# Optimization experiments

Measured on AMD Instinct MI355X. Metric: run time of the kernel, lower is better.

Reference implementation:

```python
import jax, jax.numpy as jnp
import numpy as np

NS, NM, NR, H = 5000, 100000, 2000, 128
E_SM, E_RM, E_SIM, L = 2_000_000, 1_000_000, 2_000_000, 500_000
NUM_LAYERS = 4  # flattened: layer-0 sage convs 0..3, layer-1 sage convs 0..3 -> stacked [2,4,...]


def _seg_sum(x, idx, n):
    return jax.ops.segment_sum(x, idx, num_segments=n)


def sage_conv(x_src, x_dst, Wl, bl, Wr, src, dst, n_dst):
    # PyG SAGEConv: mean-aggregate neighbor features, lin_l (with bias), + lin_r(root, no bias)
    agg = _seg_sum(x_src[src], dst, n_dst)                      # [n_dst, H]
    cnt = _seg_sum(jnp.ones_like(src, dtype=x_src.dtype), dst, n_dst)
    mean = agg / jnp.maximum(cnt, 1.0)[:, None]
    return mean @ Wl + bl + x_dst @ Wr


def gcn_conv(x, W, b, src, dst, n):
    # PyG GCNConv: add self loops, symmetric normalization deg^-1/2 (deg over dst incl. self loops)
    loop = jnp.arange(n, dtype=src.dtype)
    src2 = jnp.concatenate([src, loop])
    dst2 = jnp.concatenate([dst, loop])
    deg = _seg_sum(jnp.ones_like(dst2, dtype=x.dtype), dst2, n)
    dinv = jnp.where(deg > 0, jax.lax.rsqrt(deg), 0.0)
    norm = dinv[src2] * dinv[dst2]                               # [E+n]
    xw = x @ W                                                   # [n, H]
    out = _seg_sum(xw[src2] * norm[:, None], dst2, n)
    return out + b


def setup_inputs() -> dict:
    key = jax.random.key(0)
    ks = jax.random.split(key, 20)
    s = 0.05
    inp = {
        "emb_srna": jax.random.normal(ks[0], (NS, H), jnp.float32) * s,
        "emb_mrna": jax.random.normal(ks[1], (NM, H), jnp.float32) * s,
        "emb_rbp": jax.random.normal(ks[2], (NR, H), jnp.float32) * s,
        # stacked SAGE params: [layer=2, rel=4, ...]; rel order:
        # 0: srna->mrna, 1: mrna->srna (rev), 2: rbp->mrna, 3: mrna->rbp (rev)
        "sage_Wl": jax.random.normal(ks[3], (2, 4, H, H), jnp.float32) * s,
        "sage_bl": jnp.zeros((2, 4, H), jnp.float32),
        "sage_Wr": jax.random.normal(ks[4], (2, 4, H, H), jnp.float32) * s,
        # stacked GCN params: [layer=2, rel=2 (sim, rev_sim), ...]
        "gcn_W": jax.random.normal(ks[5], (2, 2, H, H), jnp.float32) * s,
        "gcn_b": jnp.zeros((2, 2, H), jnp.float32),
        "src_sm": jax.random.randint(ks[6], (E_SM,), 0, NS),
        "dst_sm": jax.random.randint(ks[7], (E_SM,), 0, NM),
        "src_rm": jax.random.randint(ks[8], (E_RM,), 0, NR),
        "dst_rm": jax.random.randint(ks[9], (E_RM,), 0, NM),
        "src_sim": jax.random.randint(ks[10], (E_SIM,), 0, NM),
        "dst_sim": jax.random.randint(ks[11], (E_SIM,), 0, NM),
        "lbl_srna": jax.random.randint(ks[12], (L,), 0, NS),
        "lbl_mrna": jax.random.randint(ks[13], (L,), 0, NM),
        "lbl_rbp": jax.random.randint(ks[14], (L,), 0, NR),
    }
    return inp


def reference(emb_srna, emb_mrna, emb_rbp, sage_Wl, sage_bl, sage_Wr, gcn_W, gcn_b,
              src_sm, dst_sm, src_rm, dst_rm, src_sim, dst_sim,
              lbl_srna, lbl_mrna, lbl_rbp):
    x_s, x_m, x_r = emb_srna, emb_mrna, emb_rbp
    for l in range(2):
        m_new = (
            sage_conv(x_s, x_m, sage_Wl[l, 0], sage_bl[l, 0], sage_Wr[l, 0], src_sm, dst_sm, NM)
            + sage_conv(x_r, x_m, sage_Wl[l, 2], sage_bl[l, 2], sage_Wr[l, 2], src_rm, dst_rm, NM)
            + gcn_conv(x_m, gcn_W[l, 0], gcn_b[l, 0], src_sim, dst_sim, NM)
            + gcn_conv(x_m, gcn_W[l, 1], gcn_b[l, 1], dst_sim, src_sim, NM)
        )
        s_new = sage_conv(x_m, x_s, sage_Wl[l, 1], sage_bl[l, 1], sage_Wr[l, 1], dst_sm, src_sm, NS)
        r_new = sage_conv(x_m, x_r, sage_Wl[l, 3], sage_bl[l, 3], sage_Wr[l, 3], dst_rm, src_rm, NR)
        x_s, x_m, x_r = jax.nn.relu(s_new), jax.nn.relu(m_new), jax.nn.relu(r_new)
    feat_m = x_m[lbl_mrna]
    pred_srna_mrna = jnp.sum(x_s[lbl_srna] * feat_m, axis=-1)
    pred_rbp_mrna = jnp.sum(x_r[lbl_rbp] * feat_m, axis=-1)
    return (pred_srna_mrna, pred_rbp_mrna)
```

## Files before the change

kernel.cpp:

```cpp
#include <hip/hip_runtime.h>
#include <hip/hip_bf16.h>

#define NSN 5000
#define NMN 100000
#define NRN 2000
#define HDIM 128
#define ESM 2000000
#define ERM 1000000
#define ESIM 2000000
#define LBL 500000

#define CNT_TOTAL (4 * NMN + NSN + NRN)
#define POOL_TOTAL (2 * ESM + 2 * ERM + 2 * ESIM)
#define NBTOT 1222
#define WCAP 14336
#define MAXNODES 512
#define SR_TOTAL (NSN + NRN)

#define CAP0 12288
#define CAP1 8192
#define CAP2 7168
#define CAP3 9216
#define CAP4 12288
#define CAP5 12288
#define PB0 0
#define PB1 (PB0 + 196 * CAP0)
#define PB2 (PB1 + 313 * CAP1)
#define PB3 (PB2 + 196 * CAP2)
#define PB4 (PB3 + 125 * CAP3)
#define PB5 (PB4 + 196 * CAP4)

typedef short bf16x8 __attribute__((ext_vector_type(8)));
typedef float f32x4 __attribute__((ext_vector_type(4)));
typedef float f32x2 __attribute__((ext_vector_type(2)));

__device__ __forceinline__ unsigned short f2bf(float f) {
  unsigned u = __float_as_uint(f);
  unsigned r = (u + 0x7fffu + ((u >> 16) & 1u)) >> 16;
  return (unsigned short)r;
}
__device__ __forceinline__ float bf_lo(unsigned v) { return __uint_as_float(v << 16); }
__device__ __forceinline__ float bf_hi(unsigned v) { return __uint_as_float(v & 0xffff0000u); }
__device__ __forceinline__ unsigned pack2(float x, float y) {
  return (unsigned)f2bf(x) | ((unsigned)f2bf(y) << 16);
}
__device__ __forceinline__ void unpack8(uint4 v, float* f) {
  f[0] = bf_lo(v.x); f[1] = bf_hi(v.x);
  f[2] = bf_lo(v.y); f[3] = bf_hi(v.y);
  f[4] = bf_lo(v.z); f[5] = bf_hi(v.z);
  f[6] = bf_lo(v.w); f[7] = bf_hi(v.w);
}


__global__ void zero_int(int* __restrict__ p, int n) {
  int i = blockIdx.x * blockDim.x + threadIdx.x;
  if (i < n) p[i] = 0;
}

struct BInfo { int g; int ns; int ne; };
__device__ __forceinline__ BInfo binfo(int id) {
  BInfo bi;
  if (id < 196)       { int k = id;        bi.g = 0;                   bi.ns = k << 9; bi.ne = min(bi.ns + 512, NMN); }
  else if (id < 509)  { int k = id - 196;  bi.g = NMN;                 bi.ns = k << 4; bi.ne = min(bi.ns + 16,  NSN); }
  else if (id < 705)  { int k = id - 509;  bi.g = NMN + NSN;           bi.ns = k << 9; bi.ne = min(bi.ns + 512, NMN); }
  else if (id < 830)  { int k = id - 705;  bi.g = 2 * NMN + NSN;       bi.ns = k << 4; bi.ne = min(bi.ns + 16,  NRN); }
  else if (id < 1026) { int k = id - 830;  bi.g = 2 * NMN + NSN + NRN; bi.ns = k << 9; bi.ne = min(bi.ns + 512, NMN); }
  else                { int k = id - 1026; bi.g = 3 * NMN + NSN + NRN; bi.ns = k << 9; bi.ne = min(bi.ns + 512, NMN); }
  return bi;
}

__device__ __forceinline__ int pstart(int id) {
  if (id < 196)       return PB0 + id * CAP0;
  else if (id < 509)  return PB1 + (id - 196) * CAP1;
  else if (id < 705)  return PB2 + (id - 509) * CAP2;
  else if (id < 830)  return PB3 + (id - 705) * CAP3;
  else if (id < 1026) return PB4 + (id - 830) * CAP4;
  else                return PB5 + (id - 1026) * CAP5;
}

__global__ void init_pcur(int* __restrict__ bcur) {
  int id = blockIdx.x * blockDim.x + threadIdx.x;
  if (id < NBTOT) bcur[id] = pstart(id);
}

template <int SHF, int NBF, int SHR, int NBR>
__global__ __launch_bounds__(256) void multisplit(
    const int* __restrict__ a, const int* __restrict__ b, int n,
    int* __restrict__ bcur, int bb, int2* __restrict__ stage) {
  __shared__ int hist[NBF + NBR];
  __shared__ int gpos[NBF + NBR];
  int tid = threadIdx.x;
  int base = blockIdx.x * 4096;
  for (int k = tid; k < NBF + NBR; k += 256) hist[k] = 0;
  __syncthreads();
  int dv[16], sv[16];
#pragma unroll
  for (int j = 0; j < 16; j++) {
    int idx = base + j * 256 + tid;
    if (idx < n) {
      sv[j] = a[idx]; dv[j] = b[idx];
      atomicAdd(&hist[dv[j] >> SHF], 1);
      atomicAdd(&hist[NBF + (sv[j] >> SHR)], 1);
    } else {
      dv[j] = -1;
    }
  }
  __syncthreads();
  for (int k = tid; k < NBF + NBR; k += 256) {
    int c = hist[k];
    gpos[k] = c ? atomicAdd(&bcur[bb + k], c) : 0;
  }
  __syncthreads();
#pragma unroll
  for (int j = 0; j < 16; j++) {
    if (dv[j] >= 0) {
      int s1 = atomicAdd(&gpos[dv[j] >> SHF], 1);
      stage[s1] = make_int2(dv[j], sv[j]);
      int s2 = atomicAdd(&gpos[NBF + (sv[j] >> SHR)], 1);
      stage[s2] = make_int2(sv[j], dv[j]);
    }
  }
}

__global__ void scan_counts(const int* __restrict__ bcur, int* __restrict__ bstart,
                            int* __restrict__ off_sentinel) {
  __shared__ int buf[256];
  int t = threadIdx.x;
  int base = 0;
  for (int c0 = 0; c0 < NBTOT; c0 += 256) {
    int id = c0 + t;
    int v = (id < NBTOT) ? (bcur[id] - pstart(id)) : 0;
    buf[t] = v; __syncthreads();
    for (int o = 1; o < 256; o <<= 1) {
      int a = (t >= o) ? buf[t - o] : 0;
      __syncthreads();
      buf[t] += a;
      __syncthreads();
    }
    if (id < NBTOT) bstart[id] = buf[t] - v + base;
    base += buf[255];
    __syncthreads();
  }
  if (t == 0) { bstart[NBTOT] = base; *off_sentinel = base; }
}

__global__ __launch_bounds__(256) void scatter_bucket(
    const int2* __restrict__ stage, const int* __restrict__ bstart,
    int* __restrict__ cur, int* __restrict__ off, int* __restrict__ pool) {
  __shared__ int win[WCAP];
  __shared__ int hist[MAXNODES];
  __shared__ int part[256];
  int b = blockIdx.x;
  BInfo bi = binfo(b);
  int p0 = pstart(b);
  int d0 = bstart[b];
  int sz = bstart[b + 1] - d0;
  int nn = bi.ne - bi.ns;
  int t = threadIdx.x;
  for (int k = t; k < nn; k += 256) hist[k] = 0;
  __syncthreads();
  for (int k = t; k < sz; k += 256)
    atomicAdd(&hist[stage[p0 + k].x - bi.ns], 1);
  __syncthreads();
  int a0 = (2 * t < nn) ? hist[2 * t] : 0;
  int a1 = (2 * t + 1 < nn) ? hist[2 * t + 1] : 0;
  part[t] = a0 + a1;
  __syncthreads();
  for (int o = 1; o < 256; o <<= 1) {
    int a = (t >= o) ? part[t - o] : 0;
    __syncthreads();
    part[t] += a;
    __syncthreads();
  }
  int e0 = part[t] - a0 - a1;
  int e1 = e0 + a0;
  if (2 * t < nn)     { off[bi.g + bi.ns + 2 * t] = d0 + e0; hist[2 * t] = e0; }
  if (2 * t + 1 < nn) { off[bi.g + bi.ns + 2 * t + 1] = d0 + e1; hist[2 * t + 1] = e1; }
  __syncthreads();
  if (sz <= WCAP) {
    for (int k = t; k < sz; k += 256) {
      int2 pr = stage[p0 + k];
      int slot = atomicAdd(&hist[pr.x - bi.ns], 1);
      win[slot] = pr.y;
    }
    __syncthreads();
    for (int k = t; k < sz; k += 256) pool[d0 + k] = win[k];
  } else {
    for (int k = t; k < sz; k += 256) {
      int2 pr = stage[p0 + k];
      int slot = atomicAdd(&cur[bi.g + pr.x], 1);
      pool[d0 + hist[pr.x - bi.ns] + slot] = pr.y;
    }
  }
}

__global__ void compute_dinv(const int* __restrict__ off1, const int* __restrict__ off2,
                             float* __restrict__ dinv1, float* __restrict__ dinv2, int n) {
  int v = blockIdx.x * blockDim.x + threadIdx.x;
  if (v < n) {
    dinv1[v] = rsqrtf((float)(off1[v + 1] - off1[v] + 1));
    dinv2[v] = rsqrtf((float)(off2[v + 1] - off2[v] + 1));
  }
}

__global__ void trans_weights(const float* __restrict__ sWl, const float* __restrict__ sWr,
                              const float* __restrict__ gW, unsigned short* __restrict__ wt) {
  int i = blockIdx.x * blockDim.x + threadIdx.x;
  if (i >= 18 * 16384) return;
  int mat = i >> 14, l = mat / 9, slot = mat % 9;
  int idx = i & 16383, nn = idx >> 7, kk = idx & 127;
  int s_ = kk * 128 + nn;
  float v;
  if (slot < 4)      v = sWl[((l * 4 + slot) << 14) + s_];
  else if (slot < 6) v = gW[((l * 2 + (slot - 4)) << 14) + s_];
  else if (slot == 6) v = sWr[((l * 4 + 0) << 14) + s_] + sWr[((l * 4 + 2) << 14) + s_];
  else if (slot == 7) v = sWr[((l * 4 + 1) << 14) + s_];
  else                v = sWr[((l * 4 + 3) << 14) + s_];
  wt[i] = f2bf(v);
}

__global__ void prep_bias(const float* __restrict__ sbl, const float* __restrict__ gb,
                          float* __restrict__ biasM) {
  int i = threadIdx.x;
  int l = i >> 7, j = i & 127;
  biasM[i] = sbl[(l * 4 + 0) * 128 + j] + sbl[(l * 4 + 2) * 128 + j] +
             gb[(l * 2 + 0) * 128 + j] + gb[(l * 2 + 1) * 128 + j];
}

__global__ void cast_all(const float2* __restrict__ es, const float2* __restrict__ em,
                         const float2* __restrict__ er, unsigned* __restrict__ os,
                         unsigned* __restrict__ om, unsigned* __restrict__ orr) {
  int i = blockIdx.x * blockDim.x + threadIdx.x;
  if (i < NSN * 64) { float2 v = es[i]; os[i] = pack2(v.x, v.y); }
  if (i < NMN * 64) { float2 v = em[i]; om[i] = pack2(v.x, v.y); }
  if (i < NRN * 64) { float2 v = er[i]; orr[i] = pack2(v.x, v.y); }
}


template <bool GCN>
__device__ __forceinline__ f32x2 agg_list(const char* __restrict__ xb,
                                          const int* __restrict__ pool,
                                          const float* __restrict__ dinv,
                                          int s, int e, int l4) {
  f32x2 a0 = (f32x2)(0.f), a1 = (f32x2)(0.f);
  if (e <= s) return a0;
  for (int i0 = s; i0 < e; i0 += 64) {
    int cnt = min(64, e - i0);
    int pidx = min(i0 + (l4 >> 2), e - 1);
    int pv = pool[pidx];
    float dvv = 0.f;
    if (GCN) dvv = dinv[pv];
    int k = 0;
    for (; k + 16 <= cnt; k += 16) {
      unsigned vv[16];
      float sc[16];
#pragma unroll
      for (int j = 0; j < 16; j++) {
        int u = __builtin_amdgcn_readlane(pv, k + j);
        if (GCN)
          sc[j] = __uint_as_float(
              (unsigned)__builtin_amdgcn_readlane((int)__float_as_uint(dvv), k + j));
        vv[j] = *(const unsigned*)(xb + (((unsigned)u << 8) + (unsigned)l4));
      }
#pragma unroll
      for (int j = 0; j < 16; j++) {
        float m = GCN ? sc[j] : 1.0f;
        if (j & 1) {
          a1.x = fmaf(bf_lo(vv[j]), m, a1.x);
          a1.y = fmaf(bf_hi(vv[j]), m, a1.y);
        } else {
          a0.x = fmaf(bf_lo(vv[j]), m, a0.x);
          a0.y = fmaf(bf_hi(vv[j]), m, a0.y);
        }
      }
    }
    if (k < cnt) {
      unsigned vv[16];
      float sc[16];
#pragma unroll
      for (int j = 0; j < 16; j++) {
        int kk = min(k + j, cnt - 1);
        int u = __builtin_amdgcn_readlane(pv, kk);
        float m;
        if (k + j < cnt)
          m = GCN ? __uint_as_float(
                        (unsigned)__builtin_amdgcn_readlane((int)__float_as_uint(dvv), kk))
                  : 1.0f;
        else
          m = 0.0f;
        sc[j] = m;
        vv[j] = *(const unsigned*)(xb + (((unsigned)u << 8) + (unsigned)l4));
      }
#pragma unroll
      for (int j = 0; j < 16; j++) {
        if (j & 1) {
          a1.x = fmaf(bf_lo(vv[j]), sc[j], a1.x);
          a1.y = fmaf(bf_hi(vv[j]), sc[j], a1.y);
        } else {
          a0.x = fmaf(bf_lo(vv[j]), sc[j], a0.x);
          a0.y = fmaf(bf_hi(vv[j]), sc[j], a0.y);
        }
      }
    }
  }
  return a0 + a1;
}

__global__ __launch_bounds__(256) void agg_all(
    const unsigned* __restrict__ xs, const unsigned* __restrict__ xm,
    const unsigned* __restrict__ xr, const int* __restrict__ pool,
    const int* __restrict__ off_sm, const int* __restrict__ off_rm,
    const int* __restrict__ off_si, const int* __restrict__ off_si2,
    const int* __restrict__ off_ms, const int* __restrict__ off_mr,
    const float* __restrict__ dinv1, const float* __restrict__ dinv2,
    unsigned* __restrict__ aggA, unsigned* __restrict__ aggB,
    unsigned* __restrict__ aggC, unsigned* __restrict__ aggD,
    unsigned* __restrict__ aggS, unsigned* __restrict__ aggR) {
  int wv = blockIdx.x * 4 + (threadIdx.x >> 6);
  wv = __builtin_amdgcn_readfirstlane(wv);
  int l = threadIdx.x & 63;
  int l4 = l << 2;

  if (wv < SR_TOTAL) {
    int node;
    const int* offp;
    unsigned* outb;
    if (wv < NSN) { node = wv; offp = off_ms; outb = aggS; }
    else          { node = wv - NSN; offp = off_mr; outb = aggR; }
    int s = offp[node], e = offp[node + 1];
    f32x2 a = agg_list<false>((const char*)xm, pool, nullptr, s, e, l4);
    float inv = (e > s) ? 1.0f / (float)(e - s) : 0.0f;
    outb[(size_t)node * 64 + l] = pack2(a.x * inv, a.y * inv);
  } else {
    int w = wv - SR_TOTAL;
    int sA = off_sm[w],  eA = off_sm[w + 1];
    int sB = off_rm[w],  eB = off_rm[w + 1];
    int sC = off_si[w],  eC = off_si[w + 1];
    int sD = off_si2[w], eD = off_si2[w + 1];
    unsigned xv = xm[(size_t)w * 64 + l];
    float dw1 = dinv1[w], dw2_ = dinv2[w];

    {
      f32x2 a = agg_list<false>((const char*)xs, pool, nullptr, sA, eA, l4);
      float inv = (eA > sA) ? 1.0f / (float)(eA - sA) : 0.0f;
      aggA[(size_t)w * 64 + l] = pack2(a.x * inv, a.y * inv);
    }
    {
      f32x2 a = agg_list<false>((const char*)xr, pool, nullptr, sB, eB, l4);
      float inv = (eB > sB) ? 1.0f / (float)(eB - sB) : 0.0f;
      aggB[(size_t)w * 64 + l] = pack2(a.x * inv, a.y * inv);
    }
    {
      f32x2 a = agg_list<true>((const char*)xm, pool, dinv1, sC, eC, l4);
      float dsq = dw1 * dw1;
      float rx = a.x * dw1 + bf_lo(xv) * dsq;
      float ry = a.y * dw1 + bf_hi(xv) * dsq;
      aggC[(size_t)w * 64 + l] = pack2(rx, ry);
    }
    {
      f32x2 a = agg_list<true>((const char*)xm, pool, dinv2, sD, eD, l4);
      float dsq = dw2_ * dw2_;
      float rx = a.x * dw2_ + bf_lo(xv) * dsq;
      float ry = a.y * dw2_ + bf_hi(xv) * dsq;
      aggD[(size_t)w * 64 + l] = pack2(rx, ry);
    }
  }
}


#define LDA 136

__global__ __launch_bounds__(256) void gemm_mfma(
    const unsigned short* __restrict__ a0, const unsigned short* __restrict__ w0,
    const unsigned short* __restrict__ a1, const unsigned short* __restrict__ w1,
    const unsigned short* __restrict__ a2, const unsigned short* __restrict__ w2,
    const unsigned short* __restrict__ a3, const unsigned short* __restrict__ w3,
    const unsigned short* __restrict__ a4, const unsigned short* __restrict__ w4,
    const float* __restrict__ bias, unsigned short* __restrict__ out, int n) {
  __shared__ __align__(16) unsigned short As[64 * LDA];
  __shared__ __align__(16) unsigned short Ws[128 * LDA];

  int tid = threadIdx.x;
  int w = tid >> 6, lane = tid & 63;
  int q = lane >> 4, c = lane & 15;
  int r0 = blockIdx.x * 64;

  const unsigned short* Ap[5] = {a0, a1, a2, a3, a4};
  const unsigned short* Wp[5] = {w0, w1, w2, w3, w4};

  float bias_v[8];
#pragma unroll
  for (int n0 = 0; n0 < 8; n0++) bias_v[n0] = bias[n0 * 16 + c];

  f32x4 acc[8];
#pragma unroll
  for (int n0 = 0; n0 < 8; n0++) acc[n0] = (f32x4){0.f, 0.f, 0.f, 0.f};

  for (int p = 0; p < 5; p++) {
    if (!Ap[p]) continue;
    __syncthreads();
    for (int j = tid; j < 2048; j += 256) {
      int row = j >> 4, colc = (j & 15) * 8;
      *(uint4*)&Ws[row * LDA + colc] = *(const uint4*)(Wp[p] + row * 128 + colc);
    }
    for (int j = tid; j < 1024; j += 256) {
      int row = j >> 4, colc = (j & 15) * 8;
      uint4 v = make_uint4(0u, 0u, 0u, 0u);
      if (r0 + row < n) v = *(const uint4*)(Ap[p] + (size_t)(r0 + row) * 128 + colc);
      *(uint4*)&As[row * LDA + colc] = v;
    }
    __syncthreads();

    int arow = (w * 16 + c) * LDA;
#pragma unroll
    for (int k0 = 0; k0 < 128; k0 += 32) {
      bf16x8 af = *(const bf16x8*)&As[arow + k0 + q * 8];
#pragma unroll
      for (int n0 = 0; n0 < 8; n0++) {
        bf16x8 bfv = *(const bf16x8*)&Ws[(n0 * 16 + c) * LDA + k0 + q * 8];
        acc[n0] = __builtin_amdgcn_mfma_f32_16x16x32_bf16(af, bfv, acc[n0], 0, 0, 0);
      }
    }
  }

  __syncthreads();
#pragma unroll
  for (int n0 = 0; n0 < 8; n0++) {
#pragma unroll
    for (int reg = 0; reg < 4; reg++) {
      float v = acc[n0][reg] + bias_v[n0];
      v = fmaxf(v, 0.f);
      As[(w * 16 + q * 4 + reg) * LDA + n0 * 16 + c] = f2bf(v);
    }
  }
  __syncthreads();
  for (int j = tid; j < 1024; j += 256) {
    int row = j >> 4, colc = (j & 15) * 8;
    if (r0 + row < n)
      *(uint4*)(out + (size_t)(r0 + row) * 128 + colc) = *(const uint4*)&As[row * LDA + colc];
  }
}


__global__ void dots_kernel(const unsigned* __restrict__ xs, const unsigned* __restrict__ xm,
                            const unsigned* __restrict__ xr, const int* __restrict__ ls,
                            const int* __restrict__ lm, const int* __restrict__ lr,
                            float* __restrict__ out) {
  int wv = (blockIdx.x * blockDim.x + threadIdx.x) >> 6;
  int lane = threadIdx.x & 63;
  int q = lane >> 4, h = lane & 15;
  int i = wv * 4 + q;
  if (i >= LBL) return;
  int im = lm[i], is = ls[i], ir = lr[i];
  uint4 mv = *(const uint4*)(xm + (size_t)im * 64 + h * 4);
  uint4 sv = *(const uint4*)(xs + (size_t)is * 64 + h * 4);
  uint4 rv = *(const uint4*)(xr + (size_t)ir * 64 + h * 4);
  float fm[8], fs[8], fr[8];
  unpack8(mv, fm); unpack8(sv, fs); unpack8(rv, fr);
  float p1 = 0.f, p2 = 0.f;
#pragma unroll
  for (int j = 0; j < 8; j++) { p1 = fmaf(fs[j], fm[j], p1); p2 = fmaf(fr[j], fm[j], p2); }
#pragma unroll
  for (int m = 1; m < 16; m <<= 1) {
    p1 += __shfl_xor(p1, m, 64);
    p2 += __shfl_xor(p2, m, 64);
  }
  if (h == 0) { out[i] = p1; out[LBL + i] = p2; }
}


extern "C" void kernel_launch(void* const* d_in, const int* in_sizes, int n_in,
                              void* d_out, int out_size, void* d_ws, size_t ws_size,
                              hipStream_t stream) {
  const float* emb_s = (const float*)d_in[0];
  const float* emb_m = (const float*)d_in[1];
  const float* emb_r = (const float*)d_in[2];
  const float* sWl = (const float*)d_in[3];
  const float* sbl = (const float*)d_in[4];
  const float* sWr = (const float*)d_in[5];
  const float* gW  = (const float*)d_in[6];
  const float* gb  = (const float*)d_in[7];
  const int* src_sm  = (const int*)d_in[8];
  const int* dst_sm  = (const int*)d_in[9];
  const int* src_rm  = (const int*)d_in[10];
  const int* dst_rm  = (const int*)d_in[11];
  const int* src_sim = (const int*)d_in[12];
  const int* dst_sim = (const int*)d_in[13];
  const int* lbl_s = (const int*)d_in[14];
  const int* lbl_m = (const int*)d_in[15];
  const int* lbl_r = (const int*)d_in[16];
  float* out = (float*)d_out;

  char* p = (char*)d_ws;
  auto alloc = [&](size_t bytes) -> char* {
    char* r = p;
    p += (bytes + 255) & ~(size_t)255;
    return r;
  };

  int* cnt_base = (int*)alloc(sizeof(int) * CNT_TOTAL);

  int* off_base = (int*)alloc(sizeof(int) * (CNT_TOTAL + 1));
  int* off_sm  = off_base;
  int* off_ms  = off_sm + NMN;
  int* off_rm  = off_ms + NSN;
  int* off_mr  = off_rm + NMN;
  int* off_si  = off_mr + NRN;
  int* off_si2 = off_si + NMN;

  int* bstart = (int*)alloc(sizeof(int) * 1280);
  int* bcur   = (int*)alloc(sizeof(int) * 1280);
  int* pool = (int*)alloc(sizeof(int) * POOL_TOTAL);

  float* dinv1 = (float*)alloc(sizeof(float) * NMN);
  float* dinv2 = (float*)alloc(sizeof(float) * NMN);

  unsigned* xsb = (unsigned*)alloc(sizeof(unsigned) * (size_t)NSN * 64);
  unsigned* xmb = (unsigned*)alloc(sizeof(unsigned) * (size_t)NMN * 64);
  unsigned* xrb = (unsigned*)alloc(sizeof(unsigned) * (size_t)NRN * 64);
  unsigned* xs0 = (unsigned*)alloc(sizeof(unsigned) * (size_t)NSN * 64);
  unsigned* xs1 = (unsigned*)alloc(sizeof(unsigned) * (size_t)NSN * 64);
  unsigned* xm0 = (unsigned*)alloc(sizeof(unsigned) * (size_t)NMN * 64);
  unsigned* xm1 = (unsigned*)alloc(sizeof(unsigned) * (size_t)NMN * 64);
  unsigned* xr0 = (unsigned*)alloc(sizeof(unsigned) * (size_t)NRN * 64);
  unsigned* xr1 = (unsigned*)alloc(sizeof(unsigned) * (size_t)NRN * 64);
  unsigned* aggA = (unsigned*)alloc(sizeof(unsigned) * (size_t)NMN * 64);
  unsigned* aggB = (unsigned*)alloc(sizeof(unsigned) * (size_t)NMN * 64);
  unsigned* aggC = (unsigned*)alloc(sizeof(unsigned) * (size_t)NMN * 64);
  unsigned* aggD = (unsigned*)alloc(sizeof(unsigned) * (size_t)NMN * 64);
  unsigned* aggS = (unsigned*)alloc(sizeof(unsigned) * (size_t)NSN * 64);
  unsigned* aggR = (unsigned*)alloc(sizeof(unsigned) * (size_t)NRN * 64);

  unsigned short* wt = (unsigned short*)alloc(sizeof(unsigned short) * 18 * 16384);
  float* biasM = (float*)alloc(sizeof(float) * 2 * 128);

  int2* stage = (int2*)aggA;

  auto WT = [&](int l, int slot) -> const unsigned short* {
    return wt + (((size_t)l * 9 + slot) << 14);
  };

  init_pcur<<<(NBTOT + 255) / 256, 256, 0, stream>>>(bcur);
  multisplit<9, 196, 4, 313><<<(ESM + 4095) / 4096, 256, 0, stream>>>(
      src_sm, dst_sm, ESM, bcur, 0, stage);
  multisplit<9, 196, 4, 125><<<(ERM + 4095) / 4096, 256, 0, stream>>>(
      src_rm, dst_rm, ERM, bcur, 509, stage);
  multisplit<9, 196, 9, 196><<<(ESIM + 4095) / 4096, 256, 0, stream>>>(
      src_sim, dst_sim, ESIM, bcur, 830, stage);
  scan_counts<<<1, 256, 0, stream>>>(bcur, bstart, off_base + CNT_TOTAL);
  zero_int<<<(CNT_TOTAL + 255) / 256, 256, 0, stream>>>(cnt_base, CNT_TOTAL);
  scatter_bucket<<<NBTOT, 256, 0, stream>>>(stage, bstart, cnt_base, off_base, pool);

  compute_dinv<<<(NMN + 255) / 256, 256, 0, stream>>>(off_si, off_si2, dinv1, dinv2, NMN);
  trans_weights<<<(18 * 16384 + 255) / 256, 256, 0, stream>>>(sWl, sWr, gW, wt);
  prep_bias<<<1, 256, 0, stream>>>(sbl, gb, biasM);
  cast_all<<<(NMN * 64 + 255) / 256, 256, 0, stream>>>((const float2*)emb_s, (const float2*)emb_m,
                                                       (const float2*)emb_r, xsb, xmb, xrb);

  const int AGG_GRID = (SR_TOTAL + NMN) / 4;
  for (int l = 0; l < 2; ++l) {
    const unsigned* xs_c = l ? xs0 : xsb;
    const unsigned* xm_c = l ? xm0 : xmb;
    const unsigned* xr_c = l ? xr0 : xrb;
    unsigned* xs_n = l ? xs1 : xs0;
    unsigned* xm_n = l ? xm1 : xm0;
    unsigned* xr_n = l ? xr1 : xr0;

    agg_all<<<AGG_GRID, 256, 0, stream>>>(
        xs_c, xm_c, xr_c, pool, off_sm, off_rm, off_si, off_si2, off_ms, off_mr,
        dinv1, dinv2, aggA, aggB, aggC, aggD, aggS, aggR);

    gemm_mfma<<<(NMN + 63) / 64, 256, 0, stream>>>(
        (const unsigned short*)aggA, WT(l, 0), (const unsigned short*)aggB, WT(l, 2),
        (const unsigned short*)aggC, WT(l, 4), (const unsigned short*)aggD, WT(l, 5),
        (const unsigned short*)xm_c, WT(l, 6), biasM + l * 128,
        (unsigned short*)xm_n, NMN);
    gemm_mfma<<<(NSN + 63) / 64, 256, 0, stream>>>(
        (const unsigned short*)aggS, WT(l, 1), (const unsigned short*)xs_c, WT(l, 7),
        nullptr, nullptr, nullptr, nullptr, nullptr, nullptr,
        sbl + (l * 4 + 1) * 128, (unsigned short*)xs_n, NSN);
    gemm_mfma<<<(NRN + 63) / 64, 256, 0, stream>>>(
        (const unsigned short*)aggR, WT(l, 3), (const unsigned short*)xr_c, WT(l, 8),
        nullptr, nullptr, nullptr, nullptr, nullptr, nullptr,
        sbl + (l * 4 + 3) * 128, (unsigned short*)xr_n, NRN);
  }

  dots_kernel<<<(LBL * 16 + 255) / 256, 256, 0, stream>>>(xs1, xm1, xr1, lbl_s, lbl_m, lbl_r, out);
}
```

Baseline: 1.091 ms.

## Fuse neighbor aggregation into per-tile MFMA GEMM, drop intermediate agg buffers

Replaces the separate aggregation kernel and three GEMM launches per layer with one fused kernel. Each block aggregates neighbor features for its 64-row tile directly into shared memory and immediately multiplies by the relation weight, accumulating across all relations in registers. This removes the write and re-read of six bf16 aggregate buffers and cuts launches from four to one per layer. In exchange each block serializes gather and MFMA phases with barriers, loses the one-wave-per-node parallelism of the old aggregation kernel, and the small sRNA/RBP blocks with heavy fan-in may become stragglers. The staging buffer, which used to reuse aggA, now gets its own allocation.

```diff
diff --git a/kernel.cpp b/kernel.cpp
--- a/kernel.cpp
+++ b/kernel.cpp
@@ -29,6 +29,7 @@
 #define PB3 (PB2 + 196 * CAP2)
 #define PB4 (PB3 + 125 * CAP3)
 #define PB5 (PB4 + 196 * CAP4)
+#define STAGE_TOTAL (PB5 + 196 * CAP5)
 
 typedef short bf16x8 __attribute__((ext_vector_type(8)));
 typedef float f32x4 __attribute__((ext_vector_type(4)));
@@ -83,15 +84,15 @@
   if (id < NBTOT) bcur[id] = pstart(id);
 }
 
-template <int SHF, int NBF, int SHR, int NBR>
+template <int SHF, int NBF, int SHR, int NBR_>
 __global__ __launch_bounds__(256) void multisplit(
     const int* __restrict__ a, const int* __restrict__ b, int n,
     int* __restrict__ bcur, int bb, int2* __restrict__ stage) {
-  __shared__ int hist[NBF + NBR];
-  __shared__ int gpos[NBF + NBR];
+  __shared__ int hist[NBF + NBR_];
+  __shared__ int gpos[NBF + NBR_];
   int tid = threadIdx.x;
   int base = blockIdx.x * 4096;
-  for (int k = tid; k < NBF + NBR; k += 256) hist[k] = 0;
+  for (int k = tid; k < NBF + NBR_; k += 256) hist[k] = 0;
   __syncthreads();
   int dv[16], sv[16];
 #pragma unroll
@@ -106,7 +107,7 @@
     }
   }
   __syncthreads();
-  for (int k = tid; k < NBF + NBR; k += 256) {
+  for (int k = tid; k < NBF + NBR_; k += 256) {
     int c = hist[k];
     gpos[k] = c ? atomicAdd(&bcur[bb + k], c) : 0;
   }
@@ -306,124 +307,113 @@
   return a0 + a1;
 }
 
-__global__ __launch_bounds__(256) void agg_all(
+
+#define LDA 136
+#define NBS 79
+#define NBR 32
+#define NBM 1563
+#define NB_FUSED (NBS + NBR + NBM)
+
+template <bool SELF, bool GCN>
+__device__ __forceinline__ void run_phase(
+    unsigned short* As, unsigned short* Ws,
+    const unsigned* __restrict__ xsrc, const int* __restrict__ pool,
+    const int* __restrict__ offp, const float* __restrict__ dinvp,
+    const unsigned short* __restrict__ Wp, int base, int n, f32x4* acc) {
+  int tid = threadIdx.x;
+  int w = tid >> 6, lane = tid & 63;
+  int q = lane >> 4, c = lane & 15;
+  for (int j = tid; j < 2048; j += 256) {
+    int row = j >> 4, colc = (j & 15) * 8;
+    *(uint4*)&Ws[row * LDA + colc] = *(const uint4*)(Wp + row * 128 + colc);
+  }
+  for (int t = 0; t < 16; ++t) {
+    int row = w * 16 + t;
+    int node = base + row;
+    unsigned val = 0u;
+    if (node < n) {
+      if (SELF) {
+        val = xsrc[(size_t)node * 64 + lane];
+      } else {
+        int s = offp[node], e = offp[node + 1];
+        f32x2 a = agg_list<GCN>((const char*)xsrc, pool, dinvp, s, e, lane << 2);
+        if (GCN) {
+          float dw = dinvp[node];
+          unsigned xv = xsrc[(size_t)node * 64 + lane];
+          float dsq = dw * dw;
+          val = pack2(a.x * dw + bf_lo(xv) * dsq, a.y * dw + bf_hi(xv) * dsq);
+        } else {
+          float inv = (e > s) ? 1.0f / (float)(e - s) : 0.0f;
+          val = pack2(a.x * inv, a.y * inv);
+        }
+      }
+    }
+    *(unsigned*)&As[row * LDA + (lane << 1)] = val;
+  }
+  __syncthreads();
+  int arow = (w * 16 + c) * LDA;
+#pragma unroll
+  for (int k0 = 0; k0 < 128; k0 += 32) {
+    bf16x8 af = *(const bf16x8*)&As[arow + k0 + q * 8];
+#pragma unroll
+    for (int n0 = 0; n0 < 8; n0++) {
+      bf16x8 bfv = *(const bf16x8*)&Ws[(n0 * 16 + c) * LDA + k0 + q * 8];
+      acc[n0] = __builtin_amdgcn_mfma_f32_16x16x32_bf16(af, bfv, acc[n0], 0, 0, 0);
+    }
+  }
+  __syncthreads();
+}
+
+__global__ __launch_bounds__(256) void fused_layer(
     const unsigned* __restrict__ xs, const unsigned* __restrict__ xm,
     const unsigned* __restrict__ xr, const int* __restrict__ pool,
     const int* __restrict__ off_sm, const int* __restrict__ off_rm,
     const int* __restrict__ off_si, const int* __restrict__ off_si2,
     const int* __restrict__ off_ms, const int* __restrict__ off_mr,
     const float* __restrict__ dinv1, const float* __restrict__ dinv2,
-    unsigned* __restrict__ aggA, unsigned* __restrict__ aggB,
-    unsigned* __restrict__ aggC, unsigned* __restrict__ aggD,
-    unsigned* __restrict__ aggS, unsigned* __restrict__ aggR) {
-  int wv = blockIdx.x * 4 + (threadIdx.x >> 6);
-  wv = __builtin_amdgcn_readfirstlane(wv);
-  int l = threadIdx.x & 63;
-  int l4 = l << 2;
-
-  if (wv < SR_TOTAL) {
-    int node;
-    const int* offp;
-    unsigned* outb;
-    if (wv < NSN) { node = wv; offp = off_ms; outb = aggS; }
-    else          { node = wv - NSN; offp = off_mr; outb = aggR; }
-    int s = offp[node], e = offp[node + 1];
-    f32x2 a = agg_list<false>((const char*)xm, pool, nullptr, s, e, l4);
-    float inv = (e > s) ? 1.0f / (float)(e - s) : 0.0f;
-    outb[(size_t)node * 64 + l] = pack2(a.x * inv, a.y * inv);
-  } else {
-    int w = wv - SR_TOTAL;
-    int sA = off_sm[w],  eA = off_sm[w + 1];
-    int sB = off_rm[w],  eB = off_rm[w + 1];
-    int sC = off_si[w],  eC = off_si[w + 1];
-    int sD = off_si2[w], eD = off_si2[w + 1];
-    unsigned xv = xm[(size_t)w * 64 + l];
-    float dw1 = dinv1[w], dw2_ = dinv2[w];
-
-    {
-      f32x2 a = agg_list<false>((const char*)xs, pool, nullptr, sA, eA, l4);
-      float inv = (eA > sA) ? 1.0f / (float)(eA - sA) : 0.0f;
-      aggA[(size_t)w * 64 + l] = pack2(a.x * inv, a.y * inv);
-    }
-    {
-      f32x2 a = agg_list<false>((const char*)xr, pool, nullptr, sB, eB, l4);
-      float inv = (eB > sB) ? 1.0f / (float)(eB - sB) : 0.0f;
-      aggB[(size_t)w * 64 + l] = pack2(a.x * inv, a.y * inv);
-    }
-    {
-      f32x2 a = agg_list<true>((const char*)xm, pool, dinv1, sC, eC, l4);
-      float dsq = dw1 * dw1;
-      float rx = a.x * dw1 + bf_lo(xv) * dsq;
-      float ry = a.y * dw1 + bf_hi(xv) * dsq;
-      aggC[(size_t)w * 64 + l] = pack2(rx, ry);
-    }
-    {
-      f32x2 a = agg_list<true>((const char*)xm, pool, dinv2, sD, eD, l4);
-      float dsq = dw2_ * dw2_;
-      float rx = a.x * dw2_ + bf_lo(xv) * dsq;
-      float ry = a.y * dw2_ + bf_hi(xv) * dsq;
-      aggD[(size_t)w * 64 + l] = pack2(rx, ry);
-    }
-  }
-}
-
-
-#define LDA 136
-
-__global__ __launch_bounds__(256) void gemm_mfma(
-    const unsigned short* __restrict__ a0, const unsigned short* __restrict__ w0,
-    const unsigned short* __restrict__ a1, const unsigned short* __restrict__ w1,
-    const unsigned short* __restrict__ a2, const unsigned short* __restrict__ w2,
-    const unsigned short* __restrict__ a3, const unsigned short* __restrict__ w3,
-    const unsigned short* __restrict__ a4, const unsigned short* __restrict__ w4,
-    const float* __restrict__ bias, unsigned short* __restrict__ out, int n) {
+    const unsigned short* __restrict__ wt, const float* __restrict__ biasM,
+    const float* __restrict__ sbl, int layer,
+    unsigned short* __restrict__ xs_n, unsigned short* __restrict__ xm_n,
+    unsigned short* __restrict__ xr_n) {
   __shared__ __align__(16) unsigned short As[64 * LDA];
   __shared__ __align__(16) unsigned short Ws[128 * LDA];
-
-  int tid = threadIdx.x;
+  int b = blockIdx.x, tid = threadIdx.x;
   int w = tid >> 6, lane = tid & 63;
   int q = lane >> 4, c = lane & 15;
-  int r0 = blockIdx.x * 64;
-
-  const unsigned short* Ap[5] = {a0, a1, a2, a3, a4};
-  const unsigned short* Wp[5] = {w0, w1, w2, w3, w4};
+
+  f32x4 acc[8];
+#pragma unroll
+  for (int n0 = 0; n0 < 8; n0++) acc[n0] = (f32x4){0.f, 0.f, 0.f, 0.f};
+
+  const unsigned short* wbase = wt + (((size_t)layer * 9) << 14);
+  int base, n;
+  unsigned short* outp;
+  const float* bias;
+
+  if (b < NBS) {
+    base = b * 64; n = NSN; outp = xs_n;
+    bias = sbl + (layer * 4 + 1) * 128;
+    run_phase<false, false>(As, Ws, xm, pool, off_ms, nullptr, wbase + (1 << 14), base, n, acc);
+    run_phase<true,  false>(As, Ws, xs, pool, nullptr, nullptr, wbase + (7 << 14), base, n, acc);
+  } else if (b < NBS + NBR) {
+    base = (b - NBS) * 64; n = NRN; outp = xr_n;
+    bias = sbl + (layer * 4 + 3) * 128;
+    run_phase<false, false>(As, Ws, xm, pool, off_mr, nullptr, wbase + (3 << 14), base, n, acc);
+    run_phase<true,  false>(As, Ws, xr, pool, nullptr, nullptr, wbase + (8 << 14), base, n, acc);
+  } else {
+    base = (b - NBS - NBR) * 64; n = NMN; outp = xm_n;
+    bias = biasM + layer * 128;
+    run_phase<false, false>(As, Ws, xs, pool, off_sm,  nullptr, wbase + (0 << 14), base, n, acc);
+    run_phase<false, false>(As, Ws, xr, pool, off_rm,  nullptr, wbase + (2 << 14), base, n, acc);
+    run_phase<false, true >(As, Ws, xm, pool, off_si,  dinv1,   wbase + (4 << 14), base, n, acc);
+    run_phase<false, true >(As, Ws, xm, pool, off_si2, dinv2,   wbase + (5 << 14), base, n, acc);
+    run_phase<true,  false>(As, Ws, xm, pool, nullptr, nullptr, wbase + (6 << 14), base, n, acc);
+  }
 
   float bias_v[8];
 #pragma unroll
   for (int n0 = 0; n0 < 8; n0++) bias_v[n0] = bias[n0 * 16 + c];
 
-  f32x4 acc[8];
-#pragma unroll
-  for (int n0 = 0; n0 < 8; n0++) acc[n0] = (f32x4){0.f, 0.f, 0.f, 0.f};
-
-  for (int p = 0; p < 5; p++) {
-    if (!Ap[p]) continue;
-    __syncthreads();
-    for (int j = tid; j < 2048; j += 256) {
-      int row = j >> 4, colc = (j & 15) * 8;
-      *(uint4*)&Ws[row * LDA + colc] = *(const uint4*)(Wp[p] + row * 128 + colc);
-    }
-    for (int j = tid; j < 1024; j += 256) {
-      int row = j >> 4, colc = (j & 15) * 8;
-      uint4 v = make_uint4(0u, 0u, 0u, 0u);
-      if (r0 + row < n) v = *(const uint4*)(Ap[p] + (size_t)(r0 + row) * 128 + colc);
-      *(uint4*)&As[row * LDA + colc] = v;
-    }
-    __syncthreads();
-
-    int arow = (w * 16 + c) * LDA;
-#pragma unroll
-    for (int k0 = 0; k0 < 128; k0 += 32) {
-      bf16x8 af = *(const bf16x8*)&As[arow + k0 + q * 8];
-#pragma unroll
-      for (int n0 = 0; n0 < 8; n0++) {
-        bf16x8 bfv = *(const bf16x8*)&Ws[(n0 * 16 + c) * LDA + k0 + q * 8];
-        acc[n0] = __builtin_amdgcn_mfma_f32_16x16x32_bf16(af, bfv, acc[n0], 0, 0, 0);
-      }
-    }
-  }
-
-  __syncthreads();
 #pragma unroll
   for (int n0 = 0; n0 < 8; n0++) {
 #pragma unroll
@@ -436,8 +426,8 @@
   __syncthreads();
   for (int j = tid; j < 1024; j += 256) {
     int row = j >> 4, colc = (j & 15) * 8;
-    if (r0 + row < n)
-      *(uint4*)(out + (size_t)(r0 + row) * 128 + colc) = *(const uint4*)&As[row * LDA + colc];
+    if (base + row < n)
+      *(uint4*)(outp + (size_t)(base + row) * 128 + colc) = *(const uint4*)&As[row * LDA + colc];
   }
 }
 
@@ -524,21 +514,11 @@
   unsigned* xm1 = (unsigned*)alloc(sizeof(unsigned) * (size_t)NMN * 64);
   unsigned* xr0 = (unsigned*)alloc(sizeof(unsigned) * (size_t)NRN * 64);
   unsigned* xr1 = (unsigned*)alloc(sizeof(unsigned) * (size_t)NRN * 64);
-  unsigned* aggA = (unsigned*)alloc(sizeof(unsigned) * (size_t)NMN * 64);
-  unsigned* aggB = (unsigned*)alloc(sizeof(unsigned) * (size_t)NMN * 64);
-  unsigned* aggC = (unsigned*)alloc(sizeof(unsigned) * (size_t)NMN * 64);
-  unsigned* aggD = (unsigned*)alloc(sizeof(unsigned) * (size_t)NMN * 64);
-  unsigned* aggS = (unsigned*)alloc(sizeof(unsigned) * (size_t)NSN * 64);
-  unsigned* aggR = (unsigned*)alloc(sizeof(unsigned) * (size_t)NRN * 64);
 
   unsigned short* wt = (unsigned short*)alloc(sizeof(unsigned short) * 18 * 16384);
   float* biasM = (float*)alloc(sizeof(float) * 2 * 128);
 
-  int2* stage = (int2*)aggA;
-
-  auto WT = [&](int l, int slot) -> const unsigned short* {
-    return wt + (((size_t)l * 9 + slot) << 14);
-  };
+  int2* stage = (int2*)alloc(sizeof(int2) * (size_t)STAGE_TOTAL);
 
   init_pcur<<<(NBTOT + 255) / 256, 256, 0, stream>>>(bcur);
   multisplit<9, 196, 4, 313><<<(ESM + 4095) / 4096, 256, 0, stream>>>(
@@ -557,7 +537,6 @@
   cast_all<<<(NMN * 64 + 255) / 256, 256, 0, stream>>>((const float2*)emb_s, (const float2*)emb_m,
                                                        (const float2*)emb_r, xsb, xmb, xrb);
 
-  const int AGG_GRID = (SR_TOTAL + NMN) / 4;
   for (int l = 0; l < 2; ++l) {
     const unsigned* xs_c = l ? xs0 : xsb;
     const unsigned* xm_c = l ? xm0 : xmb;
@@ -566,23 +545,10 @@
     unsigned* xm_n = l ? xm1 : xm0;
     unsigned* xr_n = l ? xr1 : xr0;
 
-    agg_all<<<AGG_GRID, 256, 0, stream>>>(
+    fused_layer<<<NB_FUSED, 256, 0, stream>>>(
         xs_c, xm_c, xr_c, pool, off_sm, off_rm, off_si, off_si2, off_ms, off_mr,
-        dinv1, dinv2, aggA, aggB, aggC, aggD, aggS, aggR);
-
-    gemm_mfma<<<(NMN + 63) / 64, 256, 0, stream>>>(
-        (const unsigned short*)aggA, WT(l, 0), (const unsigned short*)aggB, WT(l, 2),
-        (const unsigned short*)aggC, WT(l, 4), (const unsigned short*)aggD, WT(l, 5),
-        (const unsigned short*)xm_c, WT(l, 6), biasM + l * 128,
-        (unsigned short*)xm_n, NMN);
-    gemm_mfma<<<(NSN + 63) / 64, 256, 0, stream>>>(
-        (const unsigned short*)aggS, WT(l, 1), (const unsigned short*)xs_c, WT(l, 7),
-        nullptr, nullptr, nullptr, nullptr, nullptr, nullptr,
-        sbl + (l * 4 + 1) * 128, (unsigned short*)xs_n, NSN);
-    gemm_mfma<<<(NRN + 63) / 64, 256, 0, stream>>>(
-        (const unsigned short*)aggR, WT(l, 3), (const unsigned short*)xr_c, WT(l, 8),
-        nullptr, nullptr, nullptr, nullptr, nullptr, nullptr,
-        sbl + (l * 4 + 3) * 128, (unsigned short*)xr_n, NRN);
+        dinv1, dinv2, wt, biasM, sbl, l,
+        (unsigned short*)xs_n, (unsigned short*)xm_n, (unsigned short*)xr_n);
   }
 
   dots_kernel<<<(LBL * 16 + 255) / 256, 256, 0, stream>>>(xs1, xm1, xr1, lbl_s, lbl_m, lbl_r, out);
```

New measurement: 2.498 ms. 129% more time.
